# Kernel optimization log

Measured on AMD Instinct MI355X. Metric: run time of the kernel, lower is better.

The kernel has to match this reference:

```python
import jax, jax.numpy as jnp
import numpy as np

B, T, I, H, O = 4096, 200, 2, 64, 2


def setup_inputs() -> dict:
    key = jax.random.key(0)
    ks = jax.random.split(key, 7)
    s = 1.0 / np.sqrt(H)  # PyTorch LSTM init scale
    return {
        "x": jax.random.normal(ks[0], (B, T, I), dtype=jnp.float32),
        "W_ih": jax.random.uniform(ks[1], (4 * H, I), jnp.float32, -s, s),
        "W_hh": jax.random.uniform(ks[2], (4 * H, H), jnp.float32, -s, s),
        "b_ih": jax.random.uniform(ks[3], (4 * H,), jnp.float32, -s, s),
        "b_hh": jax.random.uniform(ks[4], (4 * H,), jnp.float32, -s, s),
        "W_fc": jax.random.uniform(ks[5], (O, H), jnp.float32, -s, s),
        "b_fc": jax.random.uniform(ks[6], (O,), jnp.float32, -s, s),
    }


def reference(x, W_ih, W_hh, b_ih, b_hh, W_fc, b_fc):
    # Precompute input-to-gate projections for all timesteps in one GEMM.
    # xg: [T, B, 4H] (time-major for scan)
    xg = jnp.einsum("bti,gi->tbg", x, W_ih) + (b_ih + b_hh)

    def step(carry, xt):
        h, c = carry  # [B, H] each
        gates = xt + h @ W_hh.T  # [B, 4H]
        i_g, f_g, g_g, o_g = jnp.split(gates, 4, axis=-1)  # PyTorch order: i, f, g, o
        i = jax.nn.sigmoid(i_g)
        f = jax.nn.sigmoid(f_g)
        g = jnp.tanh(g_g)
        o = jax.nn.sigmoid(o_g)
        c = f * c + i * g
        h = o * jnp.tanh(c)
        return (h, c), None

    h0 = jnp.zeros((x.shape[0], W_hh.shape[1]), dtype=x.dtype)
    c0 = jnp.zeros_like(h0)
    (h_last, _), _ = jax.lax.scan(step, (h0, c0), xg)
    return h_last @ W_fc.T + b_fc  # [B, O]
```

## Files before the change

kernel.cpp:

```cpp
#include <hip/hip_runtime.h>
#include <hip/hip_bf16.h>


#define B_ 4096
#define T_ 200

typedef _Float16 half8 __attribute__((ext_vector_type(8)));
typedef float f32x4 __attribute__((ext_vector_type(4)));

#define K1f 1.4426950408889634f
#define K2f 2.8853900817779268f

__global__ __launch_bounds__(512) void lstm_kernel(
    const float* __restrict__ x,
    const float* __restrict__ W_ih,
    const float* __restrict__ W_hh,
    const float* __restrict__ b_ih,
    const float* __restrict__ b_hh,
    const float* __restrict__ W_fc,
    const float* __restrict__ b_fc,
    float* __restrict__ out)
{
    __shared__ float xs[16][404];
    __shared__ _Float16 hA[8][72];
    __shared__ _Float16 hB[8][72];
    __shared__ float wfc[130];

    const int tid  = threadIdx.x;
    const int lane = tid & 63;
    const int w    = tid >> 6;
    const int wq   = w & 3;
    const int cidx = lane & 15;
    const int grp  = lane >> 4;
    const int r0   = blockIdx.x * 16;

    for (int i4 = tid; i4 < 1600; i4 += 512) {
        const int row = i4 / 100;
        const int j4  = i4 - row * 100;
        reinterpret_cast<float4*>(&xs[row][0])[j4] =
            reinterpret_cast<const float4*>(x + (size_t)(r0 + row) * 400)[j4];
    }
    if (tid < 64) xs[tid >> 2][400 + (tid & 3)] = 0.f;
    for (int i = tid; i < 288; i += 512)
        reinterpret_cast<unsigned int*>(&hA[0][0])[i] = 0u;
    for (int i = tid; i < 288; i += 512)
        reinterpret_cast<unsigned int*>(&hB[0][0])[i] = 0u;
    if (tid < 130) wfc[tid] = (tid < 128) ? W_fc[tid] : b_fc[tid - 128];

    half8 bfrag[4][2];
    float wi0[4], wi1[4], bs[4];
    const int u = wq * 16 + cidx;
    #pragma unroll
    for (int m = 0; m < 4; ++m) {
        const float sc = (m == 2) ? K2f : -K1f;
        const int g = m * 64 + u;
        wi0[m] = W_ih[g * 2 + 0] * sc;
        wi1[m] = W_ih[g * 2 + 1] * sc;
        bs[m]  = (b_ih[g] + b_hh[g]) * sc;
        #pragma unroll
        for (int kt = 0; kt < 2; ++kt) {
            const float* p = W_hh + g * 64 + kt * 32 + grp * 8;
            const float4 lo = reinterpret_cast<const float4*>(p)[0];
            const float4 hi = reinterpret_cast<const float4*>(p)[1];
            half8 f;
            f[0] = (_Float16)(lo.x * sc); f[1] = (_Float16)(lo.y * sc);
            f[2] = (_Float16)(lo.z * sc); f[3] = (_Float16)(lo.w * sc);
            f[4] = (_Float16)(hi.x * sc); f[5] = (_Float16)(hi.y * sc);
            f[6] = (_Float16)(hi.z * sc); f[7] = (_Float16)(hi.w * sc);
            bfrag[m][kt] = f;
        }
    }

    const int arow = cidx >> 1;
    const int rowL = 2 * grp;
    float cst0 = 0.f, cst1 = 0.f;
    f32x4 acc[4];

    __syncthreads();

    #define ACT(pi, pf, pg, po, cst, hvout)                                    \
        {                                                                      \
            const float Ei = __builtin_amdgcn_exp2f(pi);                       \
            const float Ef = __builtin_amdgcn_exp2f(pf);                       \
            const float Eg = __builtin_amdgcn_exp2f(pg);                       \
            const float Eo = __builtin_amdgcn_exp2f(po);                       \
            const float fEf = 1.0f + Ef;                                       \
            const float P   = (1.0f + Ei) * (Eg + 1.0f);                       \
            const float r1  = __builtin_amdgcn_rcpf(P * fEf);                  \
            cst = fmaf(cst, P, (Eg - 1.0f) * fEf) * r1;                        \
            const float Ec = __builtin_amdgcn_exp2f(fminf(K2f * cst, 60.0f));  \
            const float r2 = __builtin_amdgcn_rcpf((1.0f + Eo) * (Ec + 1.0f)); \
            hvout = (Ec - 1.0f) * r2;                                          \
        }

    #define PHASE0(hX, gbase, t)                                               \
        {                                                                      \
            const half8 a0 = *reinterpret_cast<const half8*>(&hX[arow][grp * 8]);      \
            const half8 a1 = *reinterpret_cast<const half8*>(&hX[arow][32 + grp * 8]); \
            const float2 xv0 = *reinterpret_cast<const float2*>(&xs[(gbase) + rowL][2 * (t)]);     \
            const float2 xv1 = *reinterpret_cast<const float2*>(&xs[(gbase) + rowL + 1][2 * (t)]); \
            _Pragma("unroll")                                                  \
            for (int m = 0; m < 4; ++m) {                                      \
                const float p0 = fmaf(xv0.y, wi1[m], fmaf(xv0.x, wi0[m], bs[m])); \
                const float p1 = fmaf(xv1.y, wi1[m], fmaf(xv1.x, wi0[m], bs[m])); \
                f32x4 c = {p0, p0, p1, p1};                                    \
                c = __builtin_amdgcn_mfma_f32_16x16x32_f16(a0, bfrag[m][0], c, 0, 0, 0); \
                c = __builtin_amdgcn_mfma_f32_16x16x32_f16(a1, bfrag[m][1], c, 0, 0, 0); \
                acc[m] = c;                                                    \
            }                                                                  \
        }

    #define PHASE1(hX)                                                         \
        {                                                                      \
            float hv0, hv1;                                                    \
            ACT(acc[0][0], acc[1][0], acc[2][0], acc[3][0], cst0, hv0);        \
            ACT(acc[0][2], acc[1][2], acc[2][2], acc[3][2], cst1, hv1);        \
            hX[rowL][u]     = (_Float16)hv0;                                   \
            hX[rowL + 1][u] = (_Float16)hv1;                                   \
        }

    if (w < 4) {
        PHASE0(hA, 0, 0);
        __syncthreads();
        for (int t = 0; t < T_; ++t) {
            PHASE1(hA);
            __syncthreads();
            PHASE0(hA, 0, t + 1);
            __syncthreads();
        }
    } else {
        __syncthreads();
        for (int t = 0; t < T_; ++t) {
            PHASE0(hB, 8, t);
            __syncthreads();
            PHASE1(hB);
            __syncthreads();
        }
    }

    if (tid < 32) {
        const int r = tid & 15;
        const int o = tid >> 4;
        const _Float16* hsrc = (r < 8) ? &hA[r][0] : &hB[r - 8][0];
        float s = wfc[128 + o];
        #pragma unroll
        for (int k = 0; k < 64; ++k)
            s = fmaf(wfc[o * 64 + k], (float)hsrc[k], s);
        out[(size_t)(r0 + r) * 2 + o] = s;
    }
}

extern "C" void kernel_launch(void* const* d_in, const int* in_sizes, int n_in,
                              void* d_out, int out_size, void* d_ws, size_t ws_size,
                              hipStream_t stream) {
    const float* x    = (const float*)d_in[0];
    const float* W_ih = (const float*)d_in[1];
    const float* W_hh = (const float*)d_in[2];
    const float* b_ih = (const float*)d_in[3];
    const float* b_hh = (const float*)d_in[4];
    const float* W_fc = (const float*)d_in[5];
    const float* b_fc = (const float*)d_in[6];
    float* out = (float*)d_out;

    lstm_kernel<<<B_ / 16, 512, 0, stream>>>(x, W_ih, W_hh, b_ih, b_hh, W_fc, b_fc, out);
}
```

Before: 119.5 us.

## Split each row-group's work across all eight waves, interleaving both halves per step

Previously waves 0-3 handled rows 0-7 and waves 4-7 rows 8-15, each wave doing the gate math for two rows while alternating between compute and idle phases. Now every wave works on both halves each half-step: it does the activation for one row of group A, then issues the MFMA for group B, and the reverse after the barrier. Each lane keeps a single cell state per group and one activation per phase, with the A-operand row rotated by the wave half. The intent is to halve the serial activation work per lane and overlap MFMA latency with transcendental work. The cost is that MFMA output lanes are partly wasted, since only one accumulator element is used.

```diff
diff --git a/kernel.cpp b/kernel.cpp
--- a/kernel.cpp
+++ b/kernel.cpp
@@ -30,8 +30,9 @@
     const int lane = tid & 63;
     const int w    = tid >> 6;
     const int wq   = w & 3;
-    const int cidx = lane & 15;
-    const int grp  = lane >> 4;
+    const int hf   = w >> 2;
+    const int c    = lane & 15;
+    const int g    = lane >> 4;
     const int r0   = blockIdx.x * 16;
 
     for (int i4 = tid; i4 < 1600; i4 += 512) {
@@ -48,18 +49,18 @@
     if (tid < 130) wfc[tid] = (tid < 128) ? W_fc[tid] : b_fc[tid - 128];
 
     half8 bfrag[4][2];
-    float wi0[4], wi1[4], bs[4];
-    const int u = wq * 16 + cidx;
+    float cw0[4], cw1[4], cbs[4];
+    const int u = wq * 16 + c;
     #pragma unroll
     for (int m = 0; m < 4; ++m) {
         const float sc = (m == 2) ? K2f : -K1f;
-        const int g = m * 64 + u;
-        wi0[m] = W_ih[g * 2 + 0] * sc;
-        wi1[m] = W_ih[g * 2 + 1] * sc;
-        bs[m]  = (b_ih[g] + b_hh[g]) * sc;
+        const int gr = m * 64 + u;
+        cw0[m] = W_ih[gr * 2 + 0] * sc;
+        cw1[m] = W_ih[gr * 2 + 1] * sc;
+        cbs[m] = (b_ih[gr] + b_hh[gr]) * sc;
         #pragma unroll
         for (int kt = 0; kt < 2; ++kt) {
-            const float* p = W_hh + g * 64 + kt * 32 + grp * 8;
+            const float* p = W_hh + gr * 64 + kt * 32 + g * 8;
             const float4 lo = reinterpret_cast<const float4*>(p)[0];
             const float4 hi = reinterpret_cast<const float4*>(p)[1];
             half8 f;
@@ -71,19 +72,20 @@
         }
     }
 
-    const int arow = cidx >> 1;
-    const int rowL = 2 * grp;
-    float cst0 = 0.f, cst1 = 0.f;
-    f32x4 acc[4];
+    const int arow = ((c >> 1) + hf) & 7;
+    const int rowL = 2 * g + hf;
+    const int g8   = g * 8;
+    float cstA = 0.f, cstB = 0.f;
+    float aA[4], aB[4];
 
     __syncthreads();
 
-    #define ACT(pi, pf, pg, po, cst, hvout)                                    \
+    #define ACT(pre, cst, hvout)                                               \
         {                                                                      \
-            const float Ei = __builtin_amdgcn_exp2f(pi);                       \
-            const float Ef = __builtin_amdgcn_exp2f(pf);                       \
-            const float Eg = __builtin_amdgcn_exp2f(pg);                       \
-            const float Eo = __builtin_amdgcn_exp2f(po);                       \
+            const float Ei = __builtin_amdgcn_exp2f(pre[0]);                   \
+            const float Ef = __builtin_amdgcn_exp2f(pre[1]);                   \
+            const float Eg = __builtin_amdgcn_exp2f(pre[2]);                   \
+            const float Eo = __builtin_amdgcn_exp2f(pre[3]);                   \
             const float fEf = 1.0f + Ef;                                       \
             const float P   = (1.0f + Ei) * (Eg + 1.0f);                       \
             const float r1  = __builtin_amdgcn_rcpf(P * fEf);                  \
@@ -93,49 +95,44 @@
             hvout = (Ec - 1.0f) * r2;                                          \
         }
 
-    #define PHASE0(hX, gbase, t)                                               \
+    #define PREFETCH(hX, xrow, t, aX)                                          \
         {                                                                      \
-            const half8 a0 = *reinterpret_cast<const half8*>(&hX[arow][grp * 8]);      \
-            const half8 a1 = *reinterpret_cast<const half8*>(&hX[arow][32 + grp * 8]); \
-            const float2 xv0 = *reinterpret_cast<const float2*>(&xs[(gbase) + rowL][2 * (t)]);     \
-            const float2 xv1 = *reinterpret_cast<const float2*>(&xs[(gbase) + rowL + 1][2 * (t)]); \
+            const half8 f0 = *reinterpret_cast<const half8*>(&hX[arow][g8]);   \
+            const half8 f1 = *reinterpret_cast<const half8*>(&hX[arow][32 + g8]); \
+            const float2 xv = *reinterpret_cast<const float2*>(&xs[xrow][2 * (t)]); \
             _Pragma("unroll")                                                  \
             for (int m = 0; m < 4; ++m) {                                      \
-                const float p0 = fmaf(xv0.y, wi1[m], fmaf(xv0.x, wi0[m], bs[m])); \
-                const float p1 = fmaf(xv1.y, wi1[m], fmaf(xv1.x, wi0[m], bs[m])); \
-                f32x4 c = {p0, p0, p1, p1};                                    \
-                c = __builtin_amdgcn_mfma_f32_16x16x32_f16(a0, bfrag[m][0], c, 0, 0, 0); \
-                c = __builtin_amdgcn_mfma_f32_16x16x32_f16(a1, bfrag[m][1], c, 0, 0, 0); \
-                acc[m] = c;                                                    \
+                const float pj = fmaf(xv.y, cw1[m], fmaf(xv.x, cw0[m], cbs[m])); \
+                f32x4 z = {pj, pj, pj, pj};                                    \
+                z = __builtin_amdgcn_mfma_f32_16x16x32_f16(f0, bfrag[m][0], z, 0, 0, 0); \
+                z = __builtin_amdgcn_mfma_f32_16x16x32_f16(f1, bfrag[m][1], z, 0, 0, 0); \
+                aX[m] = z[0];                                                  \
             }                                                                  \
         }
 
-    #define PHASE1(hX)                                                         \
-        {                                                                      \
-            float hv0, hv1;                                                    \
-            ACT(acc[0][0], acc[1][0], acc[2][0], acc[3][0], cst0, hv0);        \
-            ACT(acc[0][2], acc[1][2], acc[2][2], acc[3][2], cst1, hv1);        \
-            hX[rowL][u]     = (_Float16)hv0;                                   \
-            hX[rowL + 1][u] = (_Float16)hv1;                                   \
+    {
+        const float2 xv = *reinterpret_cast<const float2*>(&xs[rowL][0]);
+        #pragma unroll
+        for (int m = 0; m < 4; ++m)
+            aA[m] = fmaf(xv.y, cw1[m], fmaf(xv.x, cw0[m], cbs[m]));
+    }
+
+    for (int t = 0; t < T_; ++t) {
+        {
+            float hv;
+            ACT(aA, cstA, hv);
+            hA[rowL][u] = (_Float16)hv;
         }
+        PREFETCH(hB, 8 + rowL, t, aB);
+        __syncthreads();
 
-    if (w < 4) {
-        PHASE0(hA, 0, 0);
+        {
+            float hv;
+            ACT(aB, cstB, hv);
+            hB[rowL][u] = (_Float16)hv;
+        }
+        PREFETCH(hA, rowL, t + 1, aA);
         __syncthreads();
-        for (int t = 0; t < T_; ++t) {
-            PHASE1(hA);
-            __syncthreads();
-            PHASE0(hA, 0, t + 1);
-            __syncthreads();
-        }
-    } else {
-        __syncthreads();
-        for (int t = 0; t < T_; ++t) {
-            PHASE0(hB, 8, t);
-            __syncthreads();
-            PHASE1(hB);
-            __syncthreads();
-        }
     }
 
     if (tid < 32) {
```

Result: slower. 142.9 us (+19.6%).
